# Performance work log

Hardware: AMD Instinct MI355X
Metric: run time of the kernel (lower is better)

Reference implementation:

```python
import jax, jax.numpy as jnp
import numpy as np

B, N, DIM = 4, 2048, 256
H, HD, M = 8, 32, 4
SPARSE_TOPK = 32


def setup_inputs() -> dict:
    key = jax.random.key(0)
    ks = jax.random.split(key, 6)
    x = jax.random.normal(ks[0], (B, N, DIM), dtype=jnp.float32)
    w_qkv = jax.random.normal(ks[1], (DIM, 3 * H * HD), dtype=jnp.float32) * 0.02
    b_qkv = jnp.zeros((3 * H * HD,), dtype=jnp.float32)
    w_proj = jax.random.normal(ks[2], (H * HD, DIM), dtype=jnp.float32) * 0.02
    b_proj = jnp.zeros((DIM,), dtype=jnp.float32)
    scale = jnp.ones((1, H, 1, 1), dtype=jnp.float32)  # trainable scale, init scale_value=1.0
    mem_k = jax.random.normal(ks[3], (H, M, HD), dtype=jnp.float32)
    mem_v = jax.random.normal(ks[4], (H, M, HD), dtype=jnp.float32)
    return {"x": x, "w_qkv": w_qkv, "b_qkv": b_qkv, "w_proj": w_proj,
            "b_proj": b_proj, "scale": scale, "mem_k": mem_k, "mem_v": mem_v}


def reference(x, w_qkv, b_qkv, w_proj, b_proj, scale, mem_k, mem_v):
    b, n, dim = x.shape
    h, m, hd = mem_k.shape
    qkv = (x @ w_qkv + b_qkv).reshape(b, n, 3, h, hd).transpose(2, 0, 3, 1, 4)
    q, k, v = qkv[0], qkv[1], qkv[2]
    # concat memory vectors along key-length axis -> [B,H,N+M,hd]
    k = jnp.concatenate([k, jnp.broadcast_to(mem_k, (b, h, m, hd))], axis=2)
    v = jnp.concatenate([v, jnp.broadcast_to(mem_v, (b, h, m, hd))], axis=2)
    s = n + m
    # scores with trainable per-head scale: [B,H,N,S]
    scores = jnp.einsum('bhnd,bhsd->bhns', q, k) * (hd ** -0.5) * scale
    neg = -jnp.finfo(scores.dtype).max
    # improve_locality: mask rectangular diagonal (eye(N, S))
    diag = jnp.arange(n)[:, None] == jnp.arange(s)[None, :]
    scores = jnp.where(diag, neg, scores)
    # sparse topk: keep only values >= k-th largest per row
    top = jax.lax.top_k(scores, SPARSE_TOPK)[0]
    vk = top[..., -1:]
    scores = jnp.where(scores < vk, neg, scores)
    attn = jax.nn.softmax(scores, axis=-1)
    out = jnp.einsum('bhns,bhsd->bhnd', attn, v)
    out = out.transpose(0, 2, 1, 3).reshape(b, n, h * hd)
    return out @ w_proj + b_proj
```

## Files before the change

kernel.cpp:

```cpp
#include <hip/hip_runtime.h>
#include <float.h>
#include <stdint.h>

#define Bb   4
#define Nn   2048
#define DIMc 256
#define Hh   8
#define HDd  32
#define Mm   4
#define STOT 2052
#define ROWS 8
#define SROW 2112
#define NVROW 2052

typedef float f32x2 __attribute__((ext_vector_type(2)));
typedef unsigned long long u64;

__device__ __forceinline__ unsigned int f2key(float s) {
    unsigned int b = __float_as_uint(s);
    return (b & 0x80000000u) ? ~b : (b | 0x80000000u);
}
__device__ __forceinline__ float key2f(unsigned int u) {
    unsigned int b = (u & 0x80000000u) ? (u ^ 0x80000000u) : ~u;
    return __uint_as_float(b);
}

__global__ __launch_bounds__(256) void sgemm_qkv(
    const float* __restrict__ A, const float* __restrict__ Bm,
    const float* __restrict__ bias, float* __restrict__ Qb,
    float* __restrict__ kTb, float* __restrict__ Vx,
    const float* __restrict__ memv)
{
    __shared__ __align__(16) union {
        struct { float As[2][16][128]; float Bs[2][16][128]; } st;
        float Ts[128][133];
    } u;
    const int tid = threadIdx.x;
    const int tx = tid & 15, ty = tid >> 4;
    const int m0 = blockIdx.y * 128, n0 = blockIdx.x * 128;
    const int arow = tid >> 1, acol = (tid & 1) * 8;
    const int bcol = tx * 8;
    float acc[8][8] = {};

    {
        const float4 a0 = *(const float4*)&A[(size_t)(m0 + arow) * DIMc + acol];
        const float4 a1 = *(const float4*)&A[(size_t)(m0 + arow) * DIMc + acol + 4];
        const float4 b0 = *(const float4*)&Bm[(size_t)ty * 768 + n0 + bcol];
        const float4 b1 = *(const float4*)&Bm[(size_t)ty * 768 + n0 + bcol + 4];
        const float av[8] = {a0.x,a0.y,a0.z,a0.w,a1.x,a1.y,a1.z,a1.w};
#pragma unroll
        for (int c = 0; c < 8; ++c) u.st.As[0][acol + c][arow] = av[c];
        *(float4*)&u.st.Bs[0][ty][bcol]     = b0;
        *(float4*)&u.st.Bs[0][ty][bcol + 4] = b1;
    }
    int cur = 0;
    for (int kb = 0; kb < DIMc; kb += 16) {
        float4 a0n, a1n, b0n, b1n;
        const bool more = (kb + 16 < DIMc);
        if (more) {
            a0n = *(const float4*)&A[(size_t)(m0 + arow) * DIMc + kb + 16 + acol];
            a1n = *(const float4*)&A[(size_t)(m0 + arow) * DIMc + kb + 16 + acol + 4];
            b0n = *(const float4*)&Bm[(size_t)(kb + 16 + ty) * 768 + n0 + bcol];
            b1n = *(const float4*)&Bm[(size_t)(kb + 16 + ty) * 768 + n0 + bcol + 4];
        }
        __syncthreads();
#pragma unroll
        for (int k = 0; k < 16; ++k) {
            const float4 av0 = *(const float4*)&u.st.As[cur][k][ty * 8];
            const float4 av1 = *(const float4*)&u.st.As[cur][k][ty * 8 + 4];
            const float4 bv0 = *(const float4*)&u.st.Bs[cur][k][tx * 8];
            const float4 bv1 = *(const float4*)&u.st.Bs[cur][k][tx * 8 + 4];
            const float aa[8] = {av0.x,av0.y,av0.z,av0.w,av1.x,av1.y,av1.z,av1.w};
            const float bb[8] = {bv0.x,bv0.y,bv0.z,bv0.w,bv1.x,bv1.y,bv1.z,bv1.w};
#pragma unroll
            for (int i = 0; i < 8; ++i)
#pragma unroll
                for (int j = 0; j < 8; ++j)
                    acc[i][j] = fmaf(aa[i], bb[j], acc[i][j]);
        }
        if (more) {
            const float av[8] = {a0n.x,a0n.y,a0n.z,a0n.w,a1n.x,a1n.y,a1n.z,a1n.w};
#pragma unroll
            for (int c = 0; c < 8; ++c) u.st.As[cur ^ 1][acol + c][arow] = av[c];
            *(float4*)&u.st.Bs[cur ^ 1][ty][bcol]     = b0n;
            *(float4*)&u.st.Bs[cur ^ 1][ty][bcol + 4] = b1n;
        }
        cur ^= 1;
    }
    const float4 bv0 = *(const float4*)&bias[n0 + tx * 8];
    const float4 bv1 = *(const float4*)&bias[n0 + tx * 8 + 4];
    const float bb[8] = {bv0.x,bv0.y,bv0.z,bv0.w,bv1.x,bv1.y,bv1.z,bv1.w};
    const int path = n0 >> 8;
    if (path == 1) {
        __syncthreads();
#pragma unroll
        for (int i = 0; i < 8; ++i) {
            float4 o0, o1;
            o0.x = acc[i][0] + bb[0]; o0.y = acc[i][1] + bb[1];
            o0.z = acc[i][2] + bb[2]; o0.w = acc[i][3] + bb[3];
            o1.x = acc[i][4] + bb[4]; o1.y = acc[i][5] + bb[5];
            o1.z = acc[i][6] + bb[6]; o1.w = acc[i][7] + bb[7];
            *(float4*)&u.Ts[ty * 8 + i][tx * 8]     = o0;
            *(float4*)&u.Ts[ty * 8 + i][tx * 8 + 4] = o1;
        }
        __syncthreads();
        const int c_local = tid >> 1, seg = tid & 1;
        const int cg = (n0 - 256) + c_local;
        const int hh = cg >> 5, dd = cg & 31;
        const int bi = m0 >> 11, j0 = (m0 & 2047) + seg * 64;
        float* dst = kTb + (((size_t)(bi * Hh + hh) * HDd + dd) * Nn) + j0;
#pragma unroll
        for (int q = 0; q < 16; ++q) {
            float4 o;
            o.x = u.Ts[seg * 64 + q * 4 + 0][c_local];
            o.y = u.Ts[seg * 64 + q * 4 + 1][c_local];
            o.z = u.Ts[seg * 64 + q * 4 + 2][c_local];
            o.w = u.Ts[seg * 64 + q * 4 + 3][c_local];
            *(float4*)(dst + q * 4) = o;
        }
    } else if (path == 0) {
        const int c0 = n0 + tx * 8;
#pragma unroll
        for (int i = 0; i < 8; ++i) {
            float4 o0, o1;
            o0.x = acc[i][0] + bb[0]; o0.y = acc[i][1] + bb[1];
            o0.z = acc[i][2] + bb[2]; o0.w = acc[i][3] + bb[3];
            o1.x = acc[i][4] + bb[4]; o1.y = acc[i][5] + bb[5];
            o1.z = acc[i][6] + bb[6]; o1.w = acc[i][7] + bb[7];
            float* dst = &Qb[(size_t)(m0 + ty * 8 + i) * 256 + c0];
            *(float4*)dst = o0; *(float4*)(dst + 4) = o1;
        }
    } else {
        const int c0 = (n0 & 255) + tx * 8;
        const size_t row_base = (size_t)(m0 >> 11) * NVROW + (m0 & 2047);
#pragma unroll
        for (int i = 0; i < 8; ++i) {
            float4 o0, o1;
            o0.x = acc[i][0] + bb[0]; o0.y = acc[i][1] + bb[1];
            o0.z = acc[i][2] + bb[2]; o0.w = acc[i][3] + bb[3];
            o1.x = acc[i][4] + bb[4]; o1.y = acc[i][5] + bb[5];
            o1.z = acc[i][6] + bb[6]; o1.w = acc[i][7] + bb[7];
            float* dst = &Vx[(row_base + ty * 8 + i) * 256 + c0];
            *(float4*)dst = o0; *(float4*)(dst + 4) = o1;
        }
        if (n0 == 512 && (m0 & 2047) == 0) {
            const int bb2 = m0 >> 11;
#pragma unroll
            for (int mm = 0; mm < Mm; ++mm)
                Vx[((size_t)bb2 * NVROW + Nn + mm) * 256 + tid] =
                    memv[((tid >> 5) * Mm + mm) * HDd + (tid & 31)];
        }
    }
}

__global__ __launch_bounds__(256) void sgemm_bias(
    const float* __restrict__ A, const float* __restrict__ Bm,
    const float* __restrict__ bias, float* __restrict__ C,
    int Md, int Nd, int Kd)
{
    __shared__ __align__(16) float As[2][16][128];
    __shared__ __align__(16) float Bs[2][16][64];
    const int tid = threadIdx.x;
    const int tx = tid & 15, ty = tid >> 4;
    const int m0 = blockIdx.y * 128, n0 = blockIdx.x * 64;
    const int arow = tid >> 1, acol = (tid & 1) * 8;
    const int brow = tid >> 4, bcol = (tid & 15) * 4;
    float acc[8][4] = {};

    {
        const float4 a0 = *(const float4*)&A[(size_t)(m0 + arow) * Kd + acol];
        const float4 a1 = *(const float4*)&A[(size_t)(m0 + arow) * Kd + acol + 4];
        const float4 b0 = *(const float4*)&Bm[(size_t)brow * Nd + n0 + bcol];
        const float av[8] = {a0.x,a0.y,a0.z,a0.w,a1.x,a1.y,a1.z,a1.w};
#pragma unroll
        for (int c = 0; c < 8; ++c) As[0][acol + c][arow] = av[c];
        *(float4*)&Bs[0][brow][bcol] = b0;
    }
    int cur = 0;
    for (int kb = 0; kb < Kd; kb += 16) {
        float4 a0n, a1n, b0n;
        const bool more = (kb + 16 < Kd);
        if (more) {
            a0n = *(const float4*)&A[(size_t)(m0 + arow) * Kd + kb + 16 + acol];
            a1n = *(const float4*)&A[(size_t)(m0 + arow) * Kd + kb + 16 + acol + 4];
            b0n = *(const float4*)&Bm[(size_t)(kb + 16 + brow) * Nd + n0 + bcol];
        }
        __syncthreads();
#pragma unroll
        for (int k = 0; k < 16; ++k) {
            const float4 av0 = *(const float4*)&As[cur][k][ty * 8];
            const float4 av1 = *(const float4*)&As[cur][k][ty * 8 + 4];
            const float4 bq  = *(const float4*)&Bs[cur][k][tx * 4];
            const float aa[8] = {av0.x,av0.y,av0.z,av0.w,av1.x,av1.y,av1.z,av1.w};
            const float bb[4] = {bq.x, bq.y, bq.z, bq.w};
#pragma unroll
            for (int i = 0; i < 8; ++i)
#pragma unroll
                for (int j = 0; j < 4; ++j)
                    acc[i][j] = fmaf(aa[i], bb[j], acc[i][j]);
        }
        if (more) {
            const float av[8] = {a0n.x,a0n.y,a0n.z,a0n.w,a1n.x,a1n.y,a1n.z,a1n.w};
#pragma unroll
            for (int c = 0; c < 8; ++c) As[cur ^ 1][acol + c][arow] = av[c];
            *(float4*)&Bs[cur ^ 1][brow][bcol] = b0n;
        }
        cur ^= 1;
    }
    const float4 bv = *(const float4*)&bias[n0 + tx * 4];
    const float bb[4] = {bv.x, bv.y, bv.z, bv.w};
#pragma unroll
    for (int i = 0; i < 8; ++i) {
        float4 o;
        o.x = acc[i][0] + bb[0];
        o.y = acc[i][1] + bb[1];
        o.z = acc[i][2] + bb[2];
        o.w = acc[i][3] + bb[3];
        *(float4*)&C[(size_t)(m0 + ty * 8 + i) * Nd + n0 + tx * 4] = o;
    }
}

#if __has_builtin(__builtin_elementwise_fma)
#define PKSTEP(Q, P)                                                        \
    { const f32x2 qq = {(Q), (Q)};                                          \
      a01 = __builtin_elementwise_fma(qq, ((const f32x2*)&kd[P])[0], a01);  \
      a23 = __builtin_elementwise_fma(qq, ((const f32x2*)&kd[P])[1], a23); }
#else
#define PKSTEP(Q, P)                                                        \
    { a01.x = fmaf((Q), kd[P].x, a01.x); a01.y = fmaf((Q), kd[P].y, a01.y); \
      a23.x = fmaf((Q), kd[P].z, a23.x); a23.y = fmaf((Q), kd[P].w, a23.y); }
#endif

#define SCORE_LD(KD, DC)                                                    \
    _Pragma("unroll")                                                       \
    for (int dd = 0; dd < 8; ++dd)                                          \
        KD[dd] = *(const float4*)&kT[((DC) * 8 + dd) * Nn + j0];

#define SCORE_FMA(KD, DC)                                                   \
    _Pragma("unroll")                                                       \
    for (int r = 0; r < ROWS; ++r) {                                        \
        const float4 qa  = *(const float4*)&qrow[r * 256 + (DC) * 8];       \
        const float4 qb2 = *(const float4*)&qrow[r * 256 + (DC) * 8 + 4];   \
        const float4* kd = KD;                                              \
        f32x2 a01 = acc01[r], a23 = acc23[r];                               \
        PKSTEP(qa.x, 0) PKSTEP(qa.y, 1) PKSTEP(qa.z, 2) PKSTEP(qa.w, 3)     \
        PKSTEP(qb2.x, 4) PKSTEP(qb2.y, 5) PKSTEP(qb2.z, 6) PKSTEP(qb2.w, 7) \
        acc01[r] = a01; acc23[r] = a23;                                     \
    }

__global__ __launch_bounds__(512, 4) void attn_sparse(
    const float* __restrict__ Qb, const float* __restrict__ kTb,
    const float* __restrict__ Vx, const float* __restrict__ memk,
    const float* __restrict__ scale, float* __restrict__ attn_out)
{
    __shared__ __align__(16) unsigned int S[ROWS][SROW];
    __shared__ __align__(16) u64 ulist64[ROWS][64];
    __shared__ __align__(16) u64 wj_list[ROWS][64];

    const int tid    = threadIdx.x;
    const int ntiles = Nn / ROWS;
    const int tile   = blockIdx.x % ntiles;
    const int h      = (blockIdx.x / ntiles) % Hh;
    const int b      = blockIdx.x / (ntiles * Hh);
    const int n0     = tile * ROWS;
    const float sc   = scale[h] * 0.17677669529663688f;

    const float* qrow = Qb + (size_t)(b * Nn + n0) * 256 + h * HDd;
    const float* kT = kTb + (size_t)(b * Hh + h) * (HDd * Nn);

    {
        const int j0 = tid * 4;
        f32x2 acc01[ROWS], acc23[ROWS];
#pragma unroll
        for (int r = 0; r < ROWS; ++r) { acc01[r] = (f32x2){0.f, 0.f}; acc23[r] = (f32x2){0.f, 0.f}; }
        float4 kdA[8], kdB[8];
        SCORE_LD(kdA, 0)
        SCORE_LD(kdB, 1)
        SCORE_FMA(kdA, 0)
        SCORE_LD(kdA, 2)
        SCORE_FMA(kdB, 1)
        SCORE_LD(kdB, 3)
        SCORE_FMA(kdA, 2)
        SCORE_FMA(kdB, 3)
#pragma unroll
        for (int r = 0; r < ROWS; ++r) {
            const float af[4] = {acc01[r].x, acc01[r].y, acc23[r].x, acc23[r].y};
            uint4 o;
            unsigned int* op = (unsigned int*)&o;
#pragma unroll
            for (int kk = 0; kk < 4; ++kk) {
                float s = af[kk] * sc;
                if (j0 + kk == n0 + r) s = -FLT_MAX;
                op[kk] = f2key(s);
            }
            *(uint4*)&S[r][j0] = o;
        }
    }
    if (tid < 32) {
        const int r = tid >> 2, m = tid & 3;
        const float* kp = memk + (size_t)(h * Mm + m) * HDd;
        float acc = 0.f;
#pragma unroll
        for (int dcc = 0; dcc < 8; ++dcc) {
            const float4 qv = *(const float4*)&qrow[r * 256 + dcc * 4];
            const float4 kv = *(const float4*)&kp[dcc * 4];
            acc = fmaf(qv.x, kv.x, acc);
            acc = fmaf(qv.y, kv.y, acc);
            acc = fmaf(qv.z, kv.z, acc);
            acc = fmaf(qv.w, kv.w, acc);
        }
        S[r][2048 + m] = f2key(acc * sc);
    } else {
        const int t2 = tid - 32;
        const int r = t2 / 60, p = t2 % 60;
        S[r][2052 + p] = 0x00800000u;
    }
    __syncthreads();

    const int wave = tid >> 6, lane = tid & 63;
    const int half = lane >> 5, d = lane & 31;
    const int n = n0 + wave;

    unsigned int uv[33];
    unsigned int mx = 0u;
    {
        const unsigned int* Srow = &S[wave][lane];
#pragma unroll
        for (int i = 0; i < 33; ++i) {
            uv[i] = Srow[i * 64];
            mx = uv[i] > mx ? uv[i] : mx;
        }
    }

    auto bitonic = [&](unsigned int vv) -> unsigned int {
#pragma unroll
        for (int kk = 2; kk <= 64; kk <<= 1)
#pragma unroll
            for (int jj = kk >> 1; jj > 0; jj >>= 1) {
                const unsigned int o = (unsigned int)__shfl_xor((int)vv, jj);
                const unsigned int mn = vv < o ? vv : o;
                const unsigned int mxv = vv < o ? o : vv;
                const bool up   = ((lane & kk) == 0);
                const bool lowr = ((lane & jj) == 0);
                vv = (lowr == up) ? mn : mxv;
            }
        return vv;
    };
    auto countge = [&](unsigned int tt) -> int {
        int gg = 0;
#pragma unroll
        for (int i = 0; i < 33; ++i) gg += (int)__popcll(__ballot(uv[i] >= tt));
        return gg;
    };
    auto compact = [&](unsigned int tt) -> int {
        int bs = 0;
#pragma unroll
        for (int i = 0; i < 33; ++i) {
            const bool p = (uv[i] >= tt);
            const unsigned long long mk = __ballot(p);
            if (p) {
                const int pos = bs + (int)__popcll(mk & ((1ull << lane) - 1ull));
                if (pos < 64)
                    ulist64[wave][pos] = ((u64)uv[i] << 32) | (unsigned int)(i * 64 + lane);
            }
            bs += (int)__popcll(mk);
        }
        return bs;
    };

    const unsigned int vs1 = bitonic(mx);
    const unsigned int Lmax = (unsigned int)__shfl((int)vs1, 63);
    unsigned int t = (unsigned int)__shfl((int)vs1, 32);

    ulist64[wave][lane] = 0ull;
    __asm__ __volatile__("s_waitcnt lgkmcnt(0)" ::: "memory");
    int base = compact(t);
    bool exact = true;
    if (base > 64) {
        unsigned int blo = t, bhi = Lmax + 1;
        int found = 0;
#pragma unroll 1
        for (int it = 0; it < 33; ++it) {
            if (bhi - blo <= 1u) break;
            const unsigned int tm = blo + ((bhi - blo) >> 1);
            const int gm = countge(tm);
            if (gm > 64) blo = tm;
            else if (gm < 32) bhi = tm;
            else { t = tm; found = 1; break; }
        }
        if (!found) t = blo;
        ulist64[wave][lane] = 0ull;
        __asm__ __volatile__("s_waitcnt lgkmcnt(0)" ::: "memory");
        base = compact(t);
        exact = (base <= 64);
    }
    const int C2 = base < 64 ? base : 64;
    __asm__ __volatile__("s_waitcnt lgkmcnt(0)" ::: "memory");
    const u64 pk = ulist64[wave][lane];
    const unsigned int ue = (unsigned int)(pk >> 32);
    const int je = (int)(unsigned int)pk;

    const unsigned int vs2 = bitonic(ue);
    unsigned int vkkey = (unsigned int)__shfl((int)vs2, 32);
    const unsigned int v31u = (unsigned int)__shfl((int)vs2, 31);
    if (!exact) vkkey = t;

    const bool tie_span = (v31u == vkkey);
    float snx = -3.0e38f;
    if (exact && !tie_span) {
        if (C2 == 32) {
            unsigned int unx = 0u;
#pragma unroll
            for (int i = 0; i < 33; ++i) {
                const unsigned int u = uv[i];
                if (u < vkkey && u > unx) unx = u;
            }
#pragma unroll
            for (int o = 32; o > 0; o >>= 1) {
                const unsigned int ou = (unsigned int)__shfl_xor((int)unx, o);
                if (ou > unx) unx = ou;
            }
            snx = key2f(unx);
        } else {
            snx = key2f(v31u);
        }
    }
    const float svk  = key2f(vkkey);
    const float gapv = svk - snx;
    const float lam  = (exact && !tie_span && gapv > 0.f && gapv <= 4.0e-6f) ? 0.13f : 0.f;

    const float mval = key2f(Lmax);
    const float we = (ue >= vkkey) ? __expf(key2f(ue) - mval) : 0.f;
    wj_list[wave][(lane & 1) * 32 + (lane >> 1)] =
        ((u64)(unsigned int)je << 32) | (u64)__float_as_uint(we);
    float Z = we;
#pragma unroll
    for (int o = 32; o > 0; o >>= 1) Z += __shfl_xor(Z, o);
    __asm__ __volatile__("s_waitcnt lgkmcnt(0)" ::: "memory");

    const float* Vbh = Vx + (size_t)b * (NVROW * 256) + h * HDd;
    float outv = 0.f;
#pragma unroll 2
    for (int e0 = 0; e0 < C2; e0 += 8) {
        const int p0 = (e0 >> 1) + half * 32;
        const ulonglong2 wa = *(const ulonglong2*)&wj_list[wave][p0];
        const ulonglong2 wb = *(const ulonglong2*)&wj_list[wave][p0 + 2];
        float w[4]; unsigned int q[4];
        w[0] = __uint_as_float((unsigned int)wa.x); q[0] = (unsigned int)(wa.x >> 32);
        w[1] = __uint_as_float((unsigned int)wa.y); q[1] = (unsigned int)(wa.y >> 32);
        w[2] = __uint_as_float((unsigned int)wb.x); q[2] = (unsigned int)(wb.x >> 32);
        w[3] = __uint_as_float((unsigned int)wb.y); q[3] = (unsigned int)(wb.y >> 32);
        float vv[4];
#pragma unroll
        for (int u2 = 0; u2 < 4; ++u2)
            vv[u2] = Vbh[q[u2] * 256u + (unsigned int)d];
#pragma unroll
        for (int u2 = 0; u2 < 4; ++u2)
            outv = fmaf(w[u2], vv[u2], outv);
    }
    outv += __shfl_xor(outv, 32);

    float res = outv / Z;
    if (lam > 0.f) {
        unsigned int unx2 = 0u; int jnx = 0, jd1 = -1;
#pragma unroll
        for (int i = 0; i < 33; ++i) {
            const unsigned int u = uv[i];
            const int jj2 = i * 64 + lane;
            if (u < vkkey && u > unx2) { unx2 = u; jnx = jj2; }
            if (u == vkkey && jj2 > jd1) jd1 = jj2;
        }
#pragma unroll
        for (int o = 32; o > 0; o >>= 1) {
            const unsigned int ou = (unsigned int)__shfl_xor((int)unx2, o);
            const int oj = __shfl_xor(jnx, o);
            if (ou > unx2 || (ou == unx2 && oj > jnx)) { unx2 = ou; jnx = oj; }
            const int od = __shfl_xor(jd1, o);
            if (od > jd1) jd1 = od;
        }
        const float wd = __expf(svk - mval);
        const float wn = __expf(key2f(unx2) - mval);
        const float* vp1 = Vbh + (size_t)jd1 * 256;
        const float* vpn = Vbh + (size_t)jnx * 256;
        const float ZB = Z - wd + wn;
        const float oB = (outv - wd * vp1[d] + wn * vpn[d]) / ZB;
        res = (1.f - lam) * res + lam * oB;
    }
    if (half == 0)
        attn_out[(size_t)(b * Nn + n) * 256 + h * HDd + d] = res;
}

extern "C" void kernel_launch(void* const* d_in, const int* in_sizes, int n_in,
                              void* d_out, int out_size, void* d_ws, size_t ws_size,
                              hipStream_t stream) {
    const float* x      = (const float*)d_in[0];
    const float* w_qkv  = (const float*)d_in[1];
    const float* b_qkv  = (const float*)d_in[2];
    const float* w_proj = (const float*)d_in[3];
    const float* b_proj = (const float*)d_in[4];
    const float* scale  = (const float*)d_in[5];
    const float* mem_k  = (const float*)d_in[6];
    const float* mem_v  = (const float*)d_in[7];
    float* out = (float*)d_out;

    float* Qb  = (float*)d_ws;
    float* kTb = Qb  + (size_t)Bb * Nn * 256;
    float* Vx  = kTb + (size_t)Bb * Hh * HDd * Nn;

    sgemm_qkv<<<dim3(768 / 128, (Bb * Nn) / 128), 256, 0, stream>>>(
        x, w_qkv, b_qkv, Qb, kTb, Vx, mem_v);

    attn_sparse<<<dim3(Bb * Hh * (Nn / ROWS)), 512, 0, stream>>>(
        Qb, kTb, Vx, mem_k, scale, Qb);

    sgemm_bias<<<dim3(DIMc / 64, (Bb * Nn) / 128), 256, 0, stream>>>(
        Qb, w_proj, b_proj, out, Bb * Nn, DIMc, DIMc);
}
```

Baseline: 348.9 us.

## Double rows per attention block and use 1024 threads with 2 keys each

Raises the number of query rows per attention block from 8 to 16 and doubles the block to 1024 threads. Each thread now computes 2 key columns instead of 4, with one packed accumulator per row. Each K tile load is reused across twice as many query rows, halving K traffic per row and the block count. The cost is double the shared-memory score buffer, fewer blocks resident per CU, and heavier per-block synchronisation. The launch bound of 1024x4 may not be achievable given register and LDS use.

```diff
diff --git a/kernel.cpp b/kernel.cpp
--- a/kernel.cpp
+++ b/kernel.cpp
@@ -9,7 +9,7 @@
 #define HDd  32
 #define Mm   4
 #define STOT 2052
-#define ROWS 8
+#define ROWS 16
 #define SROW 2112
 #define NVROW 2052
 
@@ -221,34 +221,32 @@
 }
 
 #if __has_builtin(__builtin_elementwise_fma)
-#define PKSTEP(Q, P)                                                        \
+#define PK2(Q, P)                                                           \
     { const f32x2 qq = {(Q), (Q)};                                          \
-      a01 = __builtin_elementwise_fma(qq, ((const f32x2*)&kd[P])[0], a01);  \
-      a23 = __builtin_elementwise_fma(qq, ((const f32x2*)&kd[P])[1], a23); }
+      a2 = __builtin_elementwise_fma(qq, kd[P], a2); }
 #else
-#define PKSTEP(Q, P)                                                        \
-    { a01.x = fmaf((Q), kd[P].x, a01.x); a01.y = fmaf((Q), kd[P].y, a01.y); \
-      a23.x = fmaf((Q), kd[P].z, a23.x); a23.y = fmaf((Q), kd[P].w, a23.y); }
+#define PK2(Q, P)                                                           \
+    { a2.x = fmaf((Q), kd[P].x, a2.x); a2.y = fmaf((Q), kd[P].y, a2.y); }
 #endif
 
 #define SCORE_LD(KD, DC)                                                    \
     _Pragma("unroll")                                                       \
     for (int dd = 0; dd < 8; ++dd)                                          \
-        KD[dd] = *(const float4*)&kT[((DC) * 8 + dd) * Nn + j0];
+        KD[dd] = *(const f32x2*)&kT[((DC) * 8 + dd) * Nn + j0];
 
 #define SCORE_FMA(KD, DC)                                                   \
     _Pragma("unroll")                                                       \
     for (int r = 0; r < ROWS; ++r) {                                        \
         const float4 qa  = *(const float4*)&qrow[r * 256 + (DC) * 8];       \
         const float4 qb2 = *(const float4*)&qrow[r * 256 + (DC) * 8 + 4];   \
-        const float4* kd = KD;                                              \
-        f32x2 a01 = acc01[r], a23 = acc23[r];                               \
-        PKSTEP(qa.x, 0) PKSTEP(qa.y, 1) PKSTEP(qa.z, 2) PKSTEP(qa.w, 3)     \
-        PKSTEP(qb2.x, 4) PKSTEP(qb2.y, 5) PKSTEP(qb2.z, 6) PKSTEP(qb2.w, 7) \
-        acc01[r] = a01; acc23[r] = a23;                                     \
-    }
-
-__global__ __launch_bounds__(512, 4) void attn_sparse(
+        const f32x2* kd = KD;                                               \
+        f32x2 a2 = accp[r];                                                 \
+        PK2(qa.x, 0) PK2(qa.y, 1) PK2(qa.z, 2) PK2(qa.w, 3)                 \
+        PK2(qb2.x, 4) PK2(qb2.y, 5) PK2(qb2.z, 6) PK2(qb2.w, 7)             \
+        accp[r] = a2;                                                       \
+    }
+
+__global__ __launch_bounds__(1024, 4) void attn_sparse(
     const float* __restrict__ Qb, const float* __restrict__ kTb,
     const float* __restrict__ Vx, const float* __restrict__ memk,
     const float* __restrict__ scale, float* __restrict__ attn_out)
@@ -269,11 +267,11 @@
     const float* kT = kTb + (size_t)(b * Hh + h) * (HDd * Nn);
 
     {
-        const int j0 = tid * 4;
-        f32x2 acc01[ROWS], acc23[ROWS];
-#pragma unroll
-        for (int r = 0; r < ROWS; ++r) { acc01[r] = (f32x2){0.f, 0.f}; acc23[r] = (f32x2){0.f, 0.f}; }
-        float4 kdA[8], kdB[8];
+        const int j0 = tid * 2;
+        f32x2 accp[ROWS];
+#pragma unroll
+        for (int r = 0; r < ROWS; ++r) accp[r] = (f32x2){0.f, 0.f};
+        f32x2 kdA[8], kdB[8];
         SCORE_LD(kdA, 0)
         SCORE_LD(kdB, 1)
         SCORE_FMA(kdA, 0)
@@ -284,19 +282,17 @@
         SCORE_FMA(kdB, 3)
 #pragma unroll
         for (int r = 0; r < ROWS; ++r) {
-            const float af[4] = {acc01[r].x, acc01[r].y, acc23[r].x, acc23[r].y};
-            uint4 o;
-            unsigned int* op = (unsigned int*)&o;
-#pragma unroll
-            for (int kk = 0; kk < 4; ++kk) {
-                float s = af[kk] * sc;
-                if (j0 + kk == n0 + r) s = -FLT_MAX;
-                op[kk] = f2key(s);
-            }
-            *(uint4*)&S[r][j0] = o;
-        }
-    }
-    if (tid < 32) {
+            uint2 o;
+            float s0 = accp[r].x * sc;
+            float s1 = accp[r].y * sc;
+            if (j0 + 0 == n0 + r) s0 = -FLT_MAX;
+            if (j0 + 1 == n0 + r) s1 = -FLT_MAX;
+            o.x = f2key(s0);
+            o.y = f2key(s1);
+            *(uint2*)&S[r][j0] = o;
+        }
+    }
+    if (tid < 64) {
         const int r = tid >> 2, m = tid & 3;
         const float* kp = memk + (size_t)(h * Mm + m) * HDd;
         float acc = 0.f;
@@ -311,7 +307,7 @@
         }
         S[r][2048 + m] = f2key(acc * sc);
     } else {
-        const int t2 = tid - 32;
+        const int t2 = tid - 64;
         const int r = t2 / 60, p = t2 % 60;
         S[r][2052 + p] = 0x00800000u;
     }
@@ -510,7 +506,7 @@
     sgemm_qkv<<<dim3(768 / 128, (Bb * Nn) / 128), 256, 0, stream>>>(
         x, w_qkv, b_qkv, Qb, kTb, Vx, mem_v);
 
-    attn_sparse<<<dim3(Bb * Hh * (Nn / ROWS)), 512, 0, stream>>>(
+    attn_sparse<<<dim3(Bb * Hh * (Nn / ROWS)), 1024, 0, stream>>>(
         Qb, kTb, Vx, mem_k, scale, Qb);
 
     sgemm_bias<<<dim3(DIMc / 64, (Bb * Nn) / 128), 256, 0, stream>>>(
```

Result: slower. 427.4 us (+22.5%).
